# Kernel tuning notes

Hardware: AMD Instinct MI355X
Metric: run time of the kernel (lower is better)

## Reference

```python
import jax, jax.numpy as jnp
import numpy as np

B, CIN, COUT, K, KN, HID, HW = 16, 256, 256, 3, 4, 16, 64
PAD = K // 2
EPS = 1e-5


def setup_inputs() -> dict:
    key = jax.random.key(0)
    ks = jax.random.split(key, 6)
    x = jax.random.normal(ks[0], (B, CIN, HW, HW), dtype=jnp.float32)
    # attention MLP: 1x1 conv -> BN -> ReLU -> 1x1 conv (on 1x1 pooled maps == dense)
    w1 = jax.random.normal(ks[1], (HID, CIN), dtype=jnp.float32) * (1.0 / np.sqrt(CIN))
    bn_gamma = jnp.ones((HID,), dtype=jnp.float32)
    bn_beta = jnp.zeros((HID,), dtype=jnp.float32)
    bn_mean = jnp.zeros((HID,), dtype=jnp.float32)
    bn_var = jnp.ones((HID,), dtype=jnp.float32)
    w2 = jax.random.normal(ks[2], (KN, HID), dtype=jnp.float32) * (1.0 / np.sqrt(HID))
    # kaiming-normal fan_out: std = sqrt(2 / (Cout * k * k))
    weight = jax.random.normal(ks[3], (KN, COUT, CIN, K, K), dtype=jnp.float32) * np.sqrt(2.0 / (COUT * K * K))
    return {"x": x, "w1": w1, "bn_gamma": bn_gamma, "bn_beta": bn_beta,
            "bn_mean": bn_mean, "bn_var": bn_var, "w2": w2, "weight": weight}


def reference(x, w1, bn_gamma, bn_beta, bn_mean, bn_var, w2, weight):
    b = x.shape[0]
    # global average pool -> [B, Cin]
    pooled = jnp.mean(x, axis=(2, 3))
    h = pooled @ w1.T                                   # [B, HID]
    h = (h - bn_mean) * jax.lax.rsqrt(bn_var + EPS) * bn_gamma + bn_beta
    h = jax.nn.relu(h)
    att = jax.nn.softmax(h @ w2.T, axis=1)              # [B, KN]
    # aggregate per-sample kernels: [B, Cout, Cin, K, K]
    agg_w = jnp.einsum('bk,koijl->boijl', att, weight)
    # batched dynamic conv via batch-as-groups grouped conv
    x_g = x.reshape(1, b * CIN, x.shape[2], x.shape[3])
    w_g = agg_w.reshape(b * COUT, CIN, K, K)
    out = jax.lax.conv_general_dilated(
        x_g, w_g, window_strides=(1, 1), padding=[(PAD, PAD), (PAD, PAD)],
        dimension_numbers=('NCHW', 'OIHW', 'NCHW'), feature_group_count=b)
    return out.reshape(b, COUT, out.shape[2], out.shape[3])
```

## Files before the change

### kernel.cpp

```cpp
#include <hip/hip_runtime.h>

typedef __attribute__((ext_vector_type(8))) short bf16x8;
typedef __attribute__((ext_vector_type(4))) float f32x4;

#define AS3 __attribute__((address_space(3)))
#define AS1 __attribute__((address_space(1)))

__device__ __forceinline__ unsigned short f2bf(float f) {
  unsigned u = __float_as_uint(f);
  u += 0x7fffu + ((u >> 16) & 1u);
  return (unsigned short)(u >> 16);
}
__device__ __forceinline__ float bf2f(unsigned short v) {
  return __uint_as_float((unsigned)v << 16);
}

__global__ void transpose_kernel(const float* __restrict__ x,
                                 unsigned short* __restrict__ xTp,
                                 float* __restrict__ part) {
  __shared__ unsigned short tb[64][258];
  __shared__ float redf[4][256];
  const int blk = blockIdx.x;
  const int b = blk >> 6, y = blk & 63;
  const int t = threadIdx.x;
  const int l = t & 63, w = t >> 6;
  const int coff = l >> 4;
  const int x4 = (l & 15) << 2;
  const float* src = x + (size_t)b * 256 * 4096 + (size_t)y * 64;
#pragma unroll 4
  for (int i = 0; i < 16; ++i) {
    const int c = w * 64 + i * 4 + coff;
    const float4 v = *reinterpret_cast<const float4*>(&src[(size_t)c * 4096 + x4]);
    tb[x4 + 0][c] = f2bf(v.x);
    tb[x4 + 1][c] = f2bf(v.y);
    tb[x4 + 2][c] = f2bf(v.z);
    tb[x4 + 3][c] = f2bf(v.w);
  }
  __syncthreads();
  unsigned short* dstb = xTp + (size_t)b * (4356 * 256);
  unsigned short* dst = dstb + ((size_t)(y + 1) * 66 + 1) * 256;
  float s0 = 0.f, s1 = 0.f, s2 = 0.f, s3 = 0.f;
#pragma unroll 4
  for (int i = 0; i < 16; ++i) {
    const int xx = w * 16 + i;
    ushort2 v0 = *(const ushort2*)&tb[xx][l * 4];
    ushort2 v1 = *(const ushort2*)&tb[xx][l * 4 + 2];
    s0 += bf2f(v0.x); s1 += bf2f(v0.y); s2 += bf2f(v1.x); s3 += bf2f(v1.y);
    ushort4 v = {v0.x, v0.y, v1.x, v1.y};
    *(ushort4*)&dst[(size_t)xx * 256 + l * 4] = v;
  }
  redf[w][l * 4 + 0] = s0;
  redf[w][l * 4 + 1] = s1;
  redf[w][l * 4 + 2] = s2;
  redf[w][l * 4 + 3] = s3;
  unsigned short* rowpad = dstb + ((size_t)(y + 1) * 66) * 256;
  rowpad[t] = 0;
  rowpad[65 * 256 + t] = 0;
  if (y == 0)
    for (int xx = 0; xx < 66; ++xx) dstb[(size_t)xx * 256 + t] = 0;
  if (y == 63)
    for (int xx = 0; xx < 66; ++xx) dstb[(size_t)(65 * 66 + xx) * 256 + t] = 0;
  __syncthreads();
  part[((size_t)(b * 64 + y)) * 256 + t] =
      redf[0][t] + redf[1][t] + redf[2][t] + redf[3][t];
}

__global__ void poolfin_kernel(const float* __restrict__ part,
                               float* __restrict__ pooled) {
  const int b = blockIdx.x, c = threadIdx.x;
  float s = 0.f;
  for (int y = 0; y < 64; ++y) s += part[((size_t)(b * 64 + y)) * 256 + c];
  pooled[b * 256 + c] = s * (1.0f / 4096.0f);
}

__global__ void attn_kernel(const float* __restrict__ pooled,
                            const float* __restrict__ w1,
                            const float* __restrict__ bng,
                            const float* __restrict__ bnb,
                            const float* __restrict__ bnm,
                            const float* __restrict__ bnv,
                            const float* __restrict__ w2,
                            float* __restrict__ att) {
  __shared__ float hbuf[256];
  const int t = threadIdx.x;
  const int b = t >> 4, i = t & 15;
  float s = 0.f;
  for (int c = 0; c < 256; ++c) s += pooled[b * 256 + c] * w1[i * 256 + c];
  float h = (s - bnm[i]) * rsqrtf(bnv[i] + 1e-5f) * bng[i] + bnb[i];
  hbuf[t] = fmaxf(h, 0.f);
  __syncthreads();
  if (t < 64) {
    const int bb = t >> 2, k = t & 3;
    float l = 0.f;
    for (int j = 0; j < 16; ++j) l += hbuf[bb * 16 + j] * w2[k * 16 + j];
    float m = l;
    m = fmaxf(m, __shfl_xor(m, 1, 64));
    m = fmaxf(m, __shfl_xor(m, 2, 64));
    float e = expf(l - m);
    float sum = e;
    sum += __shfl_xor(sum, 1, 64);
    sum += __shfl_xor(sum, 2, 64);
    att[bb * 4 + k] = e / sum;
  }
}

__global__ void agg_kernel(const float* __restrict__ att,
                           const float* __restrict__ wgt,
                           unsigned short* __restrict__ agg) {
  const int o = blockIdx.x;
  const int bh = blockIdx.y;
  const int c = threadIdx.x;
  float w[4][9];
#pragma unroll
  for (int k = 0; k < 4; ++k) {
    const float* wp = wgt + ((size_t)((k << 8) + o) * 256 + c) * 9;
#pragma unroll
    for (int t = 0; t < 9; ++t) w[k][t] = wp[t];
  }
  __shared__ float attS[64];
  if (c < 64) attS[c] = att[c];
  __syncthreads();
#pragma unroll 1
  for (int b = bh * 8; b < bh * 8 + 8; ++b) {
    const float a0 = attS[b * 4 + 0], a1 = attS[b * 4 + 1];
    const float a2 = attS[b * 4 + 2], a3 = attS[b * 4 + 3];
#pragma unroll
    for (int t = 0; t < 9; ++t) {
      const float v = a0 * w[0][t] + a1 * w[1][t] + a2 * w[2][t] + a3 * w[3][t];
      agg[(((size_t)(b * 9 + t) * 256) + o) * 256 + c] = f2bf(v);
    }
  }
}

__global__ __launch_bounds__(256, 2) void conv_kernel(
    const unsigned short* __restrict__ xTp,
    const unsigned short* __restrict__ agg,
    float* __restrict__ out) {
  __shared__ unsigned short lds[448 * 32 + 4 * 128 * 32];
  AS3 char* ldsA3 = (AS3 char*)lds;
  AS3 char* ldsB3 = ((AS3 char*)lds) + 28672;

  const int bid = blockIdx.x;
  const int b = bid & 15;
  const int rest = bid >> 4;
  const int mt = rest >> 1;
  const int nh = rest & 1;
  const int p0 = mt << 8;
  const int rowA0 = mt * 264;

  const int tid = threadIdx.x;
  const int lane = tid & 63;
  const int wave = tid >> 6;
  const int wm = wave >> 1;
  const int wn = wave & 1;

  const int srow = tid >> 2;
  const int scol = ((tid & 3) ^ ((tid >> 3) & 3)) << 3;
  const int sdst = srow * 64 + (tid & 3) * 16;

  const unsigned short* xbs =
      xTp + (size_t)b * (4356 * 256) + (size_t)rowA0 * 256 + scol;
  const unsigned short* aggs =
      agg + ((size_t)(b * 9) * 256 + nh * 128 + srow) * 256 + scol;

  auto stageA = [&](int c0) {
#pragma unroll
    for (int i = 0; i < 7; ++i) {
      const int h = srow + (i << 6);
      const int hs = h > 395 ? 395 : h;
      __builtin_amdgcn_global_load_lds(
          (const AS1 void*)(xbs + (size_t)hs * 256 + c0 * 32),
          (AS3 void*)(ldsA3 + sdst + (i << 12)), 16, 0, 0);
    }
  };
  auto stageB = [&](int c02, int tap2, int slot) {
#pragma unroll
    for (int j = 0; j < 2; ++j) {
      __builtin_amdgcn_global_load_lds(
          (const AS1 void*)(aggs + tap2 * 65536 + (j << 14) + c02 * 32),
          (AS3 void*)(ldsB3 + slot * 8192 + sdst + (j << 12)), 16, 0, 0);
    }
  };

  const int l15 = lane & 15;
  const int lhi = lane >> 4;
  const int hb0 = wm * 132 + l15;
  const int rslotB = (lhi ^ ((l15 >> 1) & 3)) << 4;
  int boffs[4];
#pragma unroll
  for (int n = 0; n < 4; ++n)
    boffs[n] = 28672 + (wn * 64 + n * 16 + l15) * 64 + rslotB;

  f32x4 acc[8][4];
#pragma unroll
  for (int m = 0; m < 8; ++m)
#pragma unroll
    for (int n = 0; n < 4; ++n) acc[m][n] = (f32x4){0.f, 0.f, 0.f, 0.f};

#define LDFRAG(AF, BF, tap)                                                   \
  {                                                                           \
    const int dy_ = (tap) / 3, dx_ = (tap) % 3;                               \
    const int slotR_ = (c0 + (tap)) & 3;                                      \
    _Pragma("unroll") for (int m = 0; m < 8; ++m) {                           \
      const int h_ = hb0 + ((m >> 2) + dy_) * 66 + (m & 3) * 16 + dx_;        \
      AF[m] = *(const bf16x8*)((const char*)lds + h_ * 64 +                   \
                               ((lhi ^ ((h_ >> 1) & 3)) << 4));               \
    }                                                                         \
    _Pragma("unroll") for (int n = 0; n < 4; ++n) {                           \
      BF[n] = *(const bf16x8*)((const char*)lds + slotR_ * 8192 + boffs[n]);  \
    }                                                                         \
  }

#define STAGEBT(t)                                                \
  {                                                               \
    int c02_, tap2_;                                              \
    if ((t) <= 5) { c02_ = c0; tap2_ = (t) + 3; }                 \
    else { c02_ = c0 + 1; tap2_ = (t) - 6; }                      \
    if (c02_ > 7) { c02_ = 7; tap2_ = 8; }                        \
    stageB(c02_, tap2_, (c0 + (t) + 3) & 3);                      \
  }

#define MFMACL(AF, BF)                                                        \
  _Pragma("unroll") for (int m = 0; m < 8; ++m)                               \
  _Pragma("unroll") for (int n = 0; n < 4; ++n)                               \
      acc[m][n] =                                                             \
          __builtin_amdgcn_mfma_f32_16x16x32_bf16(AF[m], BF[n], acc[m][n], 0, 0, 0);

#define TAPITER(t, AFc, BFc, AFn, BFn, PREF)                         \
  {                                                                  \
    if ((t) > 0) {                                                   \
      asm volatile("s_waitcnt vmcnt(2)" ::: "memory");               \
      __builtin_amdgcn_s_barrier();                                  \
      __builtin_amdgcn_sched_barrier(0);                             \
    }                                                                \
    STAGEBT(t);                                                      \
    if (PREF) LDFRAG(AFn, BFn, (t) + 1);                             \
    __builtin_amdgcn_s_setprio(1);                                   \
    MFMACL(AFc, BFc);                                                \
    __builtin_amdgcn_s_setprio(0);                                   \
  }

  stageB(0, 0, 0);
  stageB(0, 1, 1);
  stageB(0, 2, 2);

#pragma unroll 1
  for (int c0 = 0; c0 < 8; ++c0) {
    bf16x8 afr0[8], afr1[8], bfr0[4], bfr1[4];
    __builtin_amdgcn_s_barrier();
    stageA(c0);
    asm volatile("s_waitcnt vmcnt(0)" ::: "memory");
    __builtin_amdgcn_s_barrier();
    __builtin_amdgcn_sched_barrier(0);
    LDFRAG(afr0, bfr0, 0);
    TAPITER(0, afr0, bfr0, afr1, bfr1, 1);
    TAPITER(1, afr1, bfr1, afr0, bfr0, 1);
    TAPITER(2, afr0, bfr0, afr1, bfr1, 1);
    TAPITER(3, afr1, bfr1, afr0, bfr0, 1);
    TAPITER(4, afr0, bfr0, afr1, bfr1, 1);
    TAPITER(5, afr1, bfr1, afr0, bfr0, 1);
    TAPITER(6, afr0, bfr0, afr1, bfr1, 1);
    TAPITER(7, afr1, bfr1, afr0, bfr0, 1);
    TAPITER(8, afr0, bfr0, afr1, bfr1, 0);
  }

#pragma unroll
  for (int m = 0; m < 8; ++m) {
    const int p = p0 + wm * 128 + (m >> 2) * 64 + (m & 3) * 16 + (lhi << 2);
#pragma unroll
    for (int n = 0; n < 4; ++n) {
      const int co = nh * 128 + wn * 64 + n * 16 + l15;
      float* dst = out + ((size_t)(b * 256 + co) << 12) + p;
      *reinterpret_cast<f32x4*>(dst) = acc[m][n];
    }
  }
}

extern "C" void kernel_launch(void* const* d_in, const int* in_sizes, int n_in,
                              void* d_out, int out_size, void* d_ws, size_t ws_size,
                              hipStream_t stream) {
  const float* x = (const float*)d_in[0];
  const float* w1 = (const float*)d_in[1];
  const float* bng = (const float*)d_in[2];
  const float* bnb = (const float*)d_in[3];
  const float* bnm = (const float*)d_in[4];
  const float* bnv = (const float*)d_in[5];
  const float* w2 = (const float*)d_in[6];
  const float* wgt = (const float*)d_in[7];
  float* out = (float*)d_out;

  char* ws = (char*)d_ws;
  const size_t xtp_bytes = (size_t)16 * 4356 * 256 * 2;
  const size_t agg_bytes = (size_t)16 * 9 * 256 * 256 * 2;
  unsigned short* xTp = (unsigned short*)ws;
  unsigned short* agg = (unsigned short*)(ws + xtp_bytes);
  float* pooled = (float*)(ws + xtp_bytes + agg_bytes);
  float* att = (float*)(ws + xtp_bytes + agg_bytes + 16384);
  float* part = (float*)(ws + xtp_bytes + agg_bytes + 20480);

  transpose_kernel<<<1024, 256, 0, stream>>>(x, xTp, part);
  poolfin_kernel<<<16, 256, 0, stream>>>(part, pooled);
  attn_kernel<<<1, 256, 0, stream>>>(pooled, w1, bng, bnb, bnm, bnv, w2, att);
  agg_kernel<<<dim3(256, 2), 256, 0, stream>>>(att, wgt, agg);
  conv_kernel<<<512, 256, 0, stream>>>(xTp, agg, out);
}
```

Measured before the change: 123.0 us.

## Double-buffer activations in LDS and load weights directly from global memory

The conv kernel stops staging the aggregated weights (B operand) through LDS. Each wave now reads its B fragments straight from global memory into registers, prefetched two taps ahead. The LDS space this frees is used to double-buffer the activation tile (A operand), so the next channel chunk is fetched while the current one is computed, and most per-tap barriers are removed. The cost is uncoalesced, latency-exposed global loads for B that are repeated by each wave, plus heavier register pressure and a waitcnt pattern that may stall on the global loads.

```diff
diff --git a/kernel.cpp b/kernel.cpp
--- a/kernel.cpp
+++ b/kernel.cpp
@@ -136,9 +136,7 @@
     const unsigned short* __restrict__ xTp,
     const unsigned short* __restrict__ agg,
     float* __restrict__ out) {
-  __shared__ unsigned short lds[448 * 32 + 4 * 128 * 32];
-  AS3 char* ldsA3 = (AS3 char*)lds;
-  AS3 char* ldsB3 = ((AS3 char*)lds) + 28672;
+  __shared__ unsigned short lds[2 * 448 * 32];
 
   const int bid = blockIdx.x;
   const int b = bid & 15;
@@ -160,36 +158,25 @@
 
   const unsigned short* xbs =
       xTp + (size_t)b * (4356 * 256) + (size_t)rowA0 * 256 + scol;
-  const unsigned short* aggs =
-      agg + ((size_t)(b * 9) * 256 + nh * 128 + srow) * 256 + scol;
-
-  auto stageA = [&](int c0) {
+  AS3 char* ldsA3 = (AS3 char*)lds;
+
+  auto stageA = [&](int c0s, int bufb) {
 #pragma unroll
     for (int i = 0; i < 7; ++i) {
       const int h = srow + (i << 6);
       const int hs = h > 395 ? 395 : h;
       __builtin_amdgcn_global_load_lds(
-          (const AS1 void*)(xbs + (size_t)hs * 256 + c0 * 32),
-          (AS3 void*)(ldsA3 + sdst + (i << 12)), 16, 0, 0);
-    }
-  };
-  auto stageB = [&](int c02, int tap2, int slot) {
-#pragma unroll
-    for (int j = 0; j < 2; ++j) {
-      __builtin_amdgcn_global_load_lds(
-          (const AS1 void*)(aggs + tap2 * 65536 + (j << 14) + c02 * 32),
-          (AS3 void*)(ldsB3 + slot * 8192 + sdst + (j << 12)), 16, 0, 0);
+          (const AS1 void*)(xbs + (size_t)hs * 256 + c0s * 32),
+          (AS3 void*)(ldsA3 + bufb + sdst + (i << 12)), 16, 0, 0);
     }
   };
 
   const int l15 = lane & 15;
   const int lhi = lane >> 4;
   const int hb0 = wm * 132 + l15;
-  const int rslotB = (lhi ^ ((l15 >> 1) & 3)) << 4;
-  int boffs[4];
-#pragma unroll
-  for (int n = 0; n < 4; ++n)
-    boffs[n] = 28672 + (wn * 64 + n * 16 + l15) * 64 + rslotB;
+
+  const unsigned short* aggb = agg + (size_t)b * 9 * 256 * 256 +
+                               (size_t)(nh * 128 + wn * 64 + l15) * 256 + lhi * 8;
 
   f32x4 acc[8][4];
 #pragma unroll
@@ -197,71 +184,58 @@
 #pragma unroll
     for (int n = 0; n < 4; ++n) acc[m][n] = (f32x4){0.f, 0.f, 0.f, 0.f};
 
-#define LDFRAG(AF, BF, tap)                                                   \
-  {                                                                           \
-    const int dy_ = (tap) / 3, dx_ = (tap) % 3;                               \
-    const int slotR_ = (c0 + (tap)) & 3;                                      \
-    _Pragma("unroll") for (int m = 0; m < 8; ++m) {                           \
-      const int h_ = hb0 + ((m >> 2) + dy_) * 66 + (m & 3) * 16 + dx_;        \
-      AF[m] = *(const bf16x8*)((const char*)lds + h_ * 64 +                   \
-                               ((lhi ^ ((h_ >> 1) & 3)) << 4));               \
-    }                                                                         \
-    _Pragma("unroll") for (int n = 0; n < 4; ++n) {                           \
-      BF[n] = *(const bf16x8*)((const char*)lds + slotR_ * 8192 + boffs[n]);  \
-    }                                                                         \
-  }
-
-#define STAGEBT(t)                                                \
-  {                                                               \
-    int c02_, tap2_;                                              \
-    if ((t) <= 5) { c02_ = c0; tap2_ = (t) + 3; }                 \
-    else { c02_ = c0 + 1; tap2_ = (t) - 6; }                      \
-    if (c02_ > 7) { c02_ = 7; tap2_ = 8; }                        \
-    stageB(c02_, tap2_, (c0 + (t) + 3) & 3);                      \
-  }
-
-#define MFMACL(AF, BF)                                                        \
-  _Pragma("unroll") for (int m = 0; m < 8; ++m)                               \
-  _Pragma("unroll") for (int n = 0; n < 4; ++n)                               \
-      acc[m][n] =                                                             \
-          __builtin_amdgcn_mfma_f32_16x16x32_bf16(AF[m], BF[n], acc[m][n], 0, 0, 0);
-
-#define TAPITER(t, AFc, BFc, AFn, BFn, PREF)                         \
-  {                                                                  \
-    if ((t) > 0) {                                                   \
-      asm volatile("s_waitcnt vmcnt(2)" ::: "memory");               \
-      __builtin_amdgcn_s_barrier();                                  \
-      __builtin_amdgcn_sched_barrier(0);                             \
-    }                                                                \
-    STAGEBT(t);                                                      \
-    if (PREF) LDFRAG(AFn, BFn, (t) + 1);                             \
-    __builtin_amdgcn_s_setprio(1);                                   \
-    MFMACL(AFc, BFc);                                                \
-    __builtin_amdgcn_s_setprio(0);                                   \
-  }
-
-  stageB(0, 0, 0);
-  stageB(0, 1, 1);
-  stageB(0, 2, 2);
+#define LDA8(AQ, tap, bufb)                                                \
+  {                                                                        \
+    const int dy_ = (tap) / 3, dx_ = (tap) % 3;                            \
+    _Pragma("unroll") for (int m = 0; m < 8; ++m) {                        \
+      const int h_ = hb0 + ((m >> 2) + dy_) * 66 + (m & 3) * 16 + dx_;     \
+      AQ[m] = *(const bf16x8*)((const char*)lds + (bufb) + h_ * 64 +       \
+                               ((lhi ^ ((h_ >> 1) & 3)) << 4));            \
+    }                                                                      \
+  }
+
+#define LDB4(BQ, tap)                                                      \
+  _Pragma("unroll") for (int n = 0; n < 4; ++n) BQ[n] =                    \
+      *(const bf16x8*)(aggb + (tap)*65536 + n * 4096 + c0 * 32);
+
+#define MFMA32(AQ, BQ)                                                     \
+  __builtin_amdgcn_s_setprio(1);                                           \
+  _Pragma("unroll") for (int m = 0; m < 8; ++m)                            \
+  _Pragma("unroll") for (int n = 0; n < 4; ++n)                            \
+      acc[m][n] = __builtin_amdgcn_mfma_f32_16x16x32_bf16(AQ[m], BQ[n],    \
+                                                          acc[m][n], 0, 0, 0); \
+  __builtin_amdgcn_s_setprio(0);
+
+#define TAP(t, AQc, BQc, AQn, PA, PB)        \
+  {                                          \
+    if (PA) LDA8(AQn, (t) + 1, bufb);        \
+    MFMA32(AQc, BQc);                        \
+    if (PB) LDB4(BQc, (t) + 2);              \
+    __builtin_amdgcn_sched_barrier(0);       \
+  }
+
+  stageA(0, 0);
 
 #pragma unroll 1
   for (int c0 = 0; c0 < 8; ++c0) {
-    bf16x8 afr0[8], afr1[8], bfr0[4], bfr1[4];
-    __builtin_amdgcn_s_barrier();
-    stageA(c0);
+    const int bufb = (c0 & 1) * 28672;
+    bf16x8 aq0[8], aq1[8], bq0[4], bq1[4];
     asm volatile("s_waitcnt vmcnt(0)" ::: "memory");
     __builtin_amdgcn_s_barrier();
     __builtin_amdgcn_sched_barrier(0);
-    LDFRAG(afr0, bfr0, 0);
-    TAPITER(0, afr0, bfr0, afr1, bfr1, 1);
-    TAPITER(1, afr1, bfr1, afr0, bfr0, 1);
-    TAPITER(2, afr0, bfr0, afr1, bfr1, 1);
-    TAPITER(3, afr1, bfr1, afr0, bfr0, 1);
-    TAPITER(4, afr0, bfr0, afr1, bfr1, 1);
-    TAPITER(5, afr1, bfr1, afr0, bfr0, 1);
-    TAPITER(6, afr0, bfr0, afr1, bfr1, 1);
-    TAPITER(7, afr1, bfr1, afr0, bfr0, 1);
-    TAPITER(8, afr0, bfr0, afr1, bfr1, 0);
+    if (c0 < 7) stageA(c0 + 1, bufb ^ 28672);
+    LDB4(bq0, 0);
+    LDB4(bq1, 1);
+    LDA8(aq0, 0, bufb);
+    TAP(0, aq0, bq0, aq1, 1, 1);
+    TAP(1, aq1, bq1, aq0, 1, 1);
+    TAP(2, aq0, bq0, aq1, 1, 1);
+    TAP(3, aq1, bq1, aq0, 1, 1);
+    TAP(4, aq0, bq0, aq1, 1, 1);
+    TAP(5, aq1, bq1, aq0, 1, 1);
+    TAP(6, aq0, bq0, aq1, 1, 1);
+    TAP(7, aq1, bq1, aq0, 1, 0);
+    TAP(8, aq0, bq0, aq1, 0, 0);
   }
 
 #pragma unroll
@@ -274,6 +248,10 @@
       *reinterpret_cast<f32x4*>(dst) = acc[m][n];
     }
   }
+#undef LDA8
+#undef LDB4
+#undef MFMA32
+#undef TAP
 }
 
 extern "C" void kernel_launch(void* const* d_in, const int* in_sizes, int n_in,
```

Result: slower. 141.6 us (+15.1%).

## Double-buffer A tile and split tap loop into half-phases with register relief

Applied to the files above, without the earlier changes.

Double-buffers the input (A) tile in LDS so the next channel chunk loads during the current chunk's taps, removing the per-chunk full vmcnt(0) stall. The B weight ring shrinks from four slots to two. Each tap now runs as two half-phases of four A fragments each, instead of prefetching a full next set of fragment registers, which cuts register pressure. LDS use rises to about 72KB, and the extra barriers per tap may cost sync overhead or lower occupancy.

```diff
diff --git a/kernel.cpp b/kernel.cpp
--- a/kernel.cpp
+++ b/kernel.cpp
@@ -136,9 +136,7 @@
     const unsigned short* __restrict__ xTp,
     const unsigned short* __restrict__ agg,
     float* __restrict__ out) {
-  __shared__ unsigned short lds[448 * 32 + 4 * 128 * 32];
-  AS3 char* ldsA3 = (AS3 char*)lds;
-  AS3 char* ldsB3 = ((AS3 char*)lds) + 28672;
+  __shared__ unsigned short lds[(2 * 448 * 32 + 2 * 128 * 32)];
 
   const int bid = blockIdx.x;
   const int b = bid & 15;
@@ -162,15 +160,17 @@
       xTp + (size_t)b * (4356 * 256) + (size_t)rowA0 * 256 + scol;
   const unsigned short* aggs =
       agg + ((size_t)(b * 9) * 256 + nh * 128 + srow) * 256 + scol;
-
-  auto stageA = [&](int c0) {
+  AS3 char* ldsA3 = (AS3 char*)lds;
+  AS3 char* ldsB3 = ((AS3 char*)lds) + 57344;
+
+  auto stageA = [&](int c0s, int bufo) {
 #pragma unroll
     for (int i = 0; i < 7; ++i) {
       const int h = srow + (i << 6);
       const int hs = h > 395 ? 395 : h;
       __builtin_amdgcn_global_load_lds(
-          (const AS1 void*)(xbs + (size_t)hs * 256 + c0 * 32),
-          (AS3 void*)(ldsA3 + sdst + (i << 12)), 16, 0, 0);
+          (const AS1 void*)(xbs + (size_t)hs * 256 + c0s * 32),
+          (AS3 void*)(ldsA3 + bufo + sdst + (i << 12)), 16, 0, 0);
     }
   };
   auto stageB = [&](int c02, int tap2, int slot) {
@@ -189,7 +189,7 @@
   int boffs[4];
 #pragma unroll
   for (int n = 0; n < 4; ++n)
-    boffs[n] = 28672 + (wn * 64 + n * 16 + l15) * 64 + rslotB;
+    boffs[n] = 57344 + (wn * 64 + n * 16 + l15) * 64 + rslotB;
 
   f32x4 acc[8][4];
 #pragma unroll
@@ -197,71 +197,64 @@
 #pragma unroll
     for (int n = 0; n < 4; ++n) acc[m][n] = (f32x4){0.f, 0.f, 0.f, 0.f};
 
-#define LDFRAG(AF, BF, tap)                                                   \
+#define RDA(reg, mm, tt)                                                      \
   {                                                                           \
-    const int dy_ = (tap) / 3, dx_ = (tap) % 3;                               \
-    const int slotR_ = (c0 + (tap)) & 3;                                      \
-    _Pragma("unroll") for (int m = 0; m < 8; ++m) {                           \
-      const int h_ = hb0 + ((m >> 2) + dy_) * 66 + (m & 3) * 16 + dx_;        \
-      AF[m] = *(const bf16x8*)((const char*)lds + h_ * 64 +                   \
-                               ((lhi ^ ((h_ >> 1) & 3)) << 4));               \
-    }                                                                         \
-    _Pragma("unroll") for (int n = 0; n < 4; ++n) {                           \
-      BF[n] = *(const bf16x8*)((const char*)lds + slotR_ * 8192 + boffs[n]);  \
-    }                                                                         \
-  }
-
-#define STAGEBT(t)                                                \
-  {                                                               \
-    int c02_, tap2_;                                              \
-    if ((t) <= 5) { c02_ = c0; tap2_ = (t) + 3; }                 \
-    else { c02_ = c0 + 1; tap2_ = (t) - 6; }                      \
-    if (c02_ > 7) { c02_ = 7; tap2_ = 8; }                        \
-    stageB(c02_, tap2_, (c0 + (t) + 3) & 3);                      \
-  }
-
-#define MFMACL(AF, BF)                                                        \
-  _Pragma("unroll") for (int m = 0; m < 8; ++m)                               \
-  _Pragma("unroll") for (int n = 0; n < 4; ++n)                               \
-      acc[m][n] =                                                             \
-          __builtin_amdgcn_mfma_f32_16x16x32_bf16(AF[m], BF[n], acc[m][n], 0, 0, 0);
-
-#define TAPITER(t, AFc, BFc, AFn, BFn, PREF)                         \
-  {                                                                  \
-    if ((t) > 0) {                                                   \
-      asm volatile("s_waitcnt vmcnt(2)" ::: "memory");               \
-      __builtin_amdgcn_s_barrier();                                  \
-      __builtin_amdgcn_sched_barrier(0);                             \
-    }                                                                \
-    STAGEBT(t);                                                      \
-    if (PREF) LDFRAG(AFn, BFn, (t) + 1);                             \
-    __builtin_amdgcn_s_setprio(1);                                   \
-    MFMACL(AFc, BFc);                                                \
-    __builtin_amdgcn_s_setprio(0);                                   \
-  }
-
+    const int h_ = hb0 + (((mm) >> 2) + (tt) / 3) * 66 + ((mm)&3) * 16 + (tt) % 3; \
+    reg = *(const bf16x8*)((const char*)lds + bufb + h_ * 64 +                \
+                           ((lhi ^ ((h_ >> 1) & 3)) << 4));                   \
+  }
+#define RDB(reg, nn, tt)                                                      \
+  reg = *(const bf16x8*)((const char*)lds + (((c0 + (tt)) & 1) << 13) + boffs[nn]);
+#define MF4(areg, ii)                                                         \
+  acc[ii][0] = __builtin_amdgcn_mfma_f32_16x16x32_bf16(areg, b0, acc[ii][0], 0, 0, 0); \
+  acc[ii][1] = __builtin_amdgcn_mfma_f32_16x16x32_bf16(areg, b1, acc[ii][1], 0, 0, 0); \
+  acc[ii][2] = __builtin_amdgcn_mfma_f32_16x16x32_bf16(areg, b2, acc[ii][2], 0, 0, 0); \
+  acc[ii][3] = __builtin_amdgcn_mfma_f32_16x16x32_bf16(areg, b3, acc[ii][3], 0, 0, 0);
+#define STB(tt)                                                               \
+  {                                                                           \
+    int c02_ = c0 + ((tt) + 2) / 9, tap2_ = ((tt) + 2) % 9;                   \
+    if (c02_ > 7) { c02_ = 7; tap2_ = 8; }                                    \
+    stageB(c02_, tap2_, (c0 + (tt)) & 1);                                     \
+  }
+#define TAPBODY(tt, VMC)                                                      \
+  {                                                                           \
+    asm volatile("s_waitcnt vmcnt(" VMC ")" ::: "memory");                    \
+    __builtin_amdgcn_s_barrier();                                             \
+    __builtin_amdgcn_sched_barrier(0);                                        \
+    bf16x8 a0, a1, a2, a3, a4, a5, a6, a7, b0, b1, b2, b3;                    \
+    RDA(a0, 0, tt) RDA(a1, 1, tt) RDA(a2, 2, tt) RDA(a3, 3, tt)               \
+    RDB(b0, 0, tt) RDB(b1, 1, tt) RDB(b2, 2, tt) RDB(b3, 3, tt)               \
+    __builtin_amdgcn_s_setprio(1);                                            \
+    MF4(a0, 0) MF4(a1, 1) MF4(a2, 2) MF4(a3, 3)                               \
+    __builtin_amdgcn_s_setprio(0);                                            \
+    __builtin_amdgcn_s_barrier();     \
+    __builtin_amdgcn_sched_barrier(0);                                        \
+    STB(tt);                                                                  \
+    if ((tt) == 0) stageA(c0 < 7 ? c0 + 1 : 7, bufb ^ 28672);                 \
+    RDA(a4, 4, tt) RDA(a5, 5, tt) RDA(a6, 6, tt) RDA(a7, 7, tt)               \
+    __builtin_amdgcn_s_setprio(1);                                            \
+    MF4(a4, 4) MF4(a5, 5) MF4(a6, 6) MF4(a7, 7)                               \
+    __builtin_amdgcn_s_setprio(0);                                            \
+  }
+
+  stageA(0, 0);
   stageB(0, 0, 0);
   stageB(0, 1, 1);
-  stageB(0, 2, 2);
+  asm volatile("s_waitcnt vmcnt(0)" ::: "memory");
+  __builtin_amdgcn_s_barrier();
 
 #pragma unroll 1
   for (int c0 = 0; c0 < 8; ++c0) {
-    bf16x8 afr0[8], afr1[8], bfr0[4], bfr1[4];
-    __builtin_amdgcn_s_barrier();
-    stageA(c0);
-    asm volatile("s_waitcnt vmcnt(0)" ::: "memory");
-    __builtin_amdgcn_s_barrier();
-    __builtin_amdgcn_sched_barrier(0);
-    LDFRAG(afr0, bfr0, 0);
-    TAPITER(0, afr0, bfr0, afr1, bfr1, 1);
-    TAPITER(1, afr1, bfr1, afr0, bfr0, 1);
-    TAPITER(2, afr0, bfr0, afr1, bfr1, 1);
-    TAPITER(3, afr1, bfr1, afr0, bfr0, 1);
-    TAPITER(4, afr0, bfr0, afr1, bfr1, 1);
-    TAPITER(5, afr1, bfr1, afr0, bfr0, 1);
-    TAPITER(6, afr0, bfr0, afr1, bfr1, 1);
-    TAPITER(7, afr1, bfr1, afr0, bfr0, 1);
-    TAPITER(8, afr0, bfr0, afr1, bfr1, 0);
+    const int bufb = (c0 & 1) * 28672;
+    TAPBODY(0, "2")
+    TAPBODY(1, "9")
+    TAPBODY(2, "9")
+    TAPBODY(3, "2")
+    TAPBODY(4, "2")
+    TAPBODY(5, "2")
+    TAPBODY(6, "2")
+    TAPBODY(7, "2")
+    TAPBODY(8, "2")
   }
 
 #pragma unroll
@@ -274,6 +267,11 @@
       *reinterpret_cast<f32x4*>(dst) = acc[m][n];
     }
   }
+#undef RDA
+#undef RDB
+#undef MF4
+#undef STB
+#undef TAPBODY
 }
 
 extern "C" void kernel_launch(void* const* d_in, const int* in_sizes, int n_in,
```

Result: slower. 130.6 us (+6.1%).
